# Optimization experiments

Hardware: AMD Instinct MI355X
Metric: run time of the kernel (lower is better)

Reference implementation:

```python
import jax, jax.numpy as jnp
import numpy as np

N = 20000        # nodes per type
E = 320000       # edges per type (avg degree 16)
H = 8            # heads
F0 = 128         # initial feature dim
F_UNI = 256      # n_unified
F_OUT = 64       # n_units per layer
N_USER = 20000   # shape_ret[0]
N_CLASSES = 2


def setup_inputs() -> dict:
    key = jax.random.key(0)
    ks = jax.random.split(key, 32)
    nrm = lambda k, s: jax.random.normal(k, s, dtype=jnp.float32) * 0.05
    inp = {
        "hemb0": nrm(ks[0], (N, F0)),
        "hemb1": nrm(ks[1], (N, F0)),
        "W0": nrm(ks[2], (F0, F_UNI)),
        "W1": nrm(ks[3], (F0, F_UNI)),
    }
    i = 4
    for t in range(2):
        for l, fin in enumerate([F_UNI, H * F_OUT]):
            inp[f"g{t}l{l}_w"] = nrm(ks[i], (H, fin, F_OUT)); i += 1
            inp[f"g{t}l{l}_asrc"] = nrm(ks[i], (H, F_OUT)); i += 1
            inp[f"g{t}l{l}_atrg"] = nrm(ks[i], (H, F_OUT)); i += 1
    inp["aw1"] = nrm(ks[i], (F_UNI, F_OUT)); i += 1
    inp["aw2"] = nrm(ks[i], (F_OUT, F_OUT)); i += 1
    inp["am"] = nrm(ks[i], (F_OUT,)); i += 1
    inp["fc_w"] = nrm(ks[i], (F_OUT * 3, N_CLASSES)); i += 1
    inp["fc_b"] = jnp.zeros((N_CLASSES,), jnp.float32); i += 1
    inp["edge0"] = jax.random.randint(ks[i], (2, E), 0, N, dtype=jnp.int32); i += 1
    inp["edge1"] = jax.random.randint(ks[i], (2, E), 0, N, dtype=jnp.int32)
    return inp


def spgat(h, src, trg, w, asrc, atrg):
    """Sparse GAT layer: h [N,f_in], edge list src/trg [E] -> [N,H,f_out]."""
    n = h.shape[0]
    hp = jnp.einsum('nf,hfo->hno', h, w)              # [H,N,O]
    s = jnp.einsum('hno,ho->nh', hp, asrc)            # [N,H]
    t = jnp.einsum('hno,ho->nh', hp, atrg)            # [N,H]
    e = jax.nn.leaky_relu(s[src] + t[trg], negative_slope=0.2)  # [E,H]
    ex = jnp.exp(e - jnp.max(e))                      # global max shift (as in source)
    denom = jax.ops.segment_sum(ex, trg, num_segments=n)[trg] + 1e-16
    alpha = ex / denom                                # [E,H]
    msg = jnp.transpose(hp, (1, 0, 2))[src] * alpha[:, :, None]  # [E,H,O]
    return jax.ops.segment_sum(msg, trg, num_segments=n)         # [N,H,O]


def reference(hemb0, hemb1, W0, W1,
              g0l0_w, g0l0_asrc, g0l0_atrg, g0l1_w, g0l1_asrc, g0l1_atrg,
              g1l0_w, g1l0_asrc, g1l0_atrg, g1l1_w, g1l1_asrc, g1l1_atrg,
              aw1, aw2, am, fc_w, fc_b, edge0, edge1):
    trans0 = hemb0 @ W0                                # [N,F_UNI]
    trans1 = hemb1 @ W1
    stacks = [
        (trans0, edge0, (g0l0_w, g0l0_asrc, g0l0_atrg), (g0l1_w, g0l1_asrc, g0l1_atrg)),
        (trans1, edge1, (g1l0_w, g1l0_asrc, g1l0_atrg), (g1l1_w, g1l1_asrc, g1l1_atrg)),
    ]
    heter = []
    for trans, edge, p0, p1 in stacks:
        src, trg = edge[0], edge[1]
        x = spgat(trans, src, trg, *p0)                # [N,H,F_OUT]
        x = jax.nn.elu(x.reshape(N, -1))               # [N,H*F_OUT]
        x = spgat(x, src, trg, *p1).mean(axis=1)       # [N,F_OUT]
        heter.append(x[:N_USER][:, None, :])
    type_aware = jnp.concatenate(heter, axis=1)        # [N_USER, 2, F_OUT]
    # faithful to source: feature = trans_emb[0] where trans_emb is the LAST
    # type's transformed embedding -> row 0, shape [F_UNI], broadcast over nodes
    feature = trans1[0]
    q = jnp.tanh(feature @ aw1 + type_aware @ aw2)     # [N_USER,2,F_OUT]
    beta = jax.nn.softmax(q @ am, axis=-1)             # [N_USER,2]
    fusion = jnp.einsum('nr,nrd->nd', beta, type_aware)[:, None, :]
    ret = jnp.concatenate([type_aware, fusion], axis=1).reshape(N_USER, -1)
    return jax.nn.log_softmax(ret @ fc_w + fc_b, axis=-1)   # [N_USER, 2]
```

## Files before the change

kernel.cpp:

```cpp
#include <hip/hip_runtime.h>
#include <hip/hip_bf16.h>


typedef __hip_bfloat16 bf16;
typedef __attribute__((ext_vector_type(8))) short short8;
typedef __attribute__((ext_vector_type(4))) float f32x4;

__device__ __forceinline__ float bf2f(bf16 v) { return __bfloat162float(v); }
__device__ __forceinline__ float ldin(const void* p, long i, int f32) {
  return f32 ? ((const float*)p)[i] : bf2f(((const bf16*)p)[i]);
}
__device__ __forceinline__ short f2bfbits(float f) {
  bf16 h = __float2bfloat16(f);
  return *reinterpret_cast<short*>(&h);
}
__device__ __forceinline__ float bfbits2f(short b) {
  unsigned u = ((unsigned)(unsigned short)b) << 16;
  return __uint_as_float(u);
}

struct GArg {
  const void* A[2];
  const void* B[2];
  bf16* C[2];
  const void* sa[2];
  const void* sb[2];
  float* sv[2];
  float* tv[2];
};

struct AArg {
  const bf16* hp[2];
  const float* sv[2];
  const float* tv[2];
  const int* rp[2];
  const int* col[2];
  void* out[2];
};

__global__ __launch_bounds__(64) void detect_kernel(const void* __restrict__ x,
                                                    int* __restrict__ flag) {
  int tid = threadIdx.x;
  float m = 0.f;
  for (int i = tid; i < 2048; i += 64) {
    float v = fabsf(bf2f(((const bf16*)x)[i]));
    if (!(v <= 1e3f)) v = 1e9f;
    m = fmaxf(m, v);
  }
#pragma unroll
  for (int off = 32; off; off >>= 1) m = fmaxf(m, __shfl_xor(m, off));
  if (tid == 0) flag[0] = (m > 1e3f) ? 1 : 0;
}

#define GBM 128
#define GBN 64
#define GBK 64

__device__ __forceinline__ int swz(int row, int kbyte) {
  return row * 128 + (kbyte ^ ((row & 7) << 4));
}

__global__ __launch_bounds__(256) void gemm_mfma(GArg g, int amode, int bmode,
                                                 int M, int K, int Nc,
                                                 const int* __restrict__ flag) {
  __shared__ bf16 As[GBM * GBK];
  __shared__ bf16 Bs[GBN * GBK];
  const int z = blockIdx.z;
  const void* __restrict__ A = g.A[z];
  const void* __restrict__ B = g.B[z];
  bf16* __restrict__ C = g.C[z];
  const void* stasrc = g.sa[z];
  const void* statrg = g.sb[z];
  float* svp = g.sv[z];
  float* tvp = g.tv[z];
  const int f32 = flag[0];
  const int af32 = (amode == 1) ? f32 : 0;
  const int m0 = blockIdx.x * GBM;
  const int n0 = blockIdx.y * GBN;
  const int tid = threadIdx.x;
  const int lane = tid & 63;
  const int wrow = (tid >> 6) * 32;

  f32x4 acc[2][4];
#pragma unroll
  for (int m = 0; m < 2; m++)
#pragma unroll
    for (int n = 0; n < 4; n++)
#pragma unroll
      for (int r = 0; r < 4; r++) acc[m][n][r] = 0.f;

  for (int kt = 0; kt < K; kt += GBK) {
#pragma unroll
    for (int j = 0; j < 4; j++) {
      int idx = tid + j * 256;
      int row = idx >> 3;
      int ks = idx & 7;
      int gm = m0 + row;
      short8 v;
#pragma unroll
      for (int e = 0; e < 8; e++) v[e] = 0;
      if (gm < M) {
        long base = (long)gm * K + kt + ks * 8;
        if (!af32) {
          v = *(const short8*)((const bf16*)A + base);
        } else {
          const float* Af = (const float*)A + base;
#pragma unroll
          for (int e = 0; e < 8; e++) v[e] = f2bfbits(Af[e]);
        }
      }
      *(short8*)((char*)As + swz(row, ks * 16)) = v;
    }
    {
      int n = tid & 63;
      int ks0 = tid >> 6;
#pragma unroll
      for (int jj = 0; jj < 2; jj++) {
        int ks = ks0 + jj * 4;
        int k = kt + ks * 8;
        int col = n0 + n;
        long base;
        int cstr;
        if (bmode == 0) { base = (long)k * Nc + col; cstr = Nc; }
        else { base = ((long)(col >> 6) * K + k) * 64 + (col & 63); cstr = 64; }
        short8 v;
        if (f32) {
          const float* Bf = (const float*)B;
#pragma unroll
          for (int e = 0; e < 8; e++) v[e] = f2bfbits(Bf[base + (long)e * cstr]);
        } else {
          const bf16* Bh = (const bf16*)B;
#pragma unroll
          for (int e = 0; e < 8; e++) v[e] = *(const short*)&Bh[base + (long)e * cstr];
        }
        *(short8*)((char*)Bs + swz(n, ks * 16)) = v;
      }
    }
    __syncthreads();
#pragma unroll
    for (int kh = 0; kh < 2; kh++) {
      int klane = kh * 64 + ((lane >> 4) << 4);
      short8 af[2], bfr[4];
#pragma unroll
      for (int m = 0; m < 2; m++) {
        int row = wrow + m * 16 + (lane & 15);
        af[m] = *(const short8*)((const char*)As + swz(row, klane));
      }
#pragma unroll
      for (int n = 0; n < 4; n++) {
        int col = n * 16 + (lane & 15);
        bfr[n] = *(const short8*)((const char*)Bs + swz(col, klane));
      }
#pragma unroll
      for (int m = 0; m < 2; m++)
#pragma unroll
        for (int n = 0; n < 4; n++)
          acc[m][n] = __builtin_amdgcn_mfma_f32_16x16x32_bf16(af[m], bfr[n], acc[m][n], 0, 0, 0);
    }
    __syncthreads();
  }
  if (svp) {
    const int h = blockIdx.y;
    const int cl = lane & 15;
    float av[4], bv[4];
#pragma unroll
    for (int n = 0; n < 4; n++) {
      av[n] = ldin(stasrc, h * 64 + n * 16 + cl, f32);
      bv[n] = ldin(statrg, h * 64 + n * 16 + cl, f32);
    }
#pragma unroll
    for (int m = 0; m < 2; m++) {
#pragma unroll
      for (int r = 0; r < 4; r++) {
        float s = 0.f, t = 0.f;
#pragma unroll
        for (int n = 0; n < 4; n++) {
          s += acc[m][n][r] * av[n];
          t += acc[m][n][r] * bv[n];
        }
#pragma unroll
        for (int off = 1; off <= 8; off <<= 1) {
          s += __shfl_xor(s, off);
          t += __shfl_xor(t, off);
        }
        int row = m0 + wrow + m * 16 + ((lane >> 4) << 2) + r;
        if (cl == 0 && row < M) {
          svp[(long)row * 8 + h] = s;
          tvp[(long)row * 8 + h] = t;
        }
      }
    }
  }
#pragma unroll
  for (int m = 0; m < 2; m++) {
#pragma unroll
    for (int r = 0; r < 4; r++) {
      int row = m0 + wrow + m * 16 + ((lane >> 4) << 2) + r;
      if (row < M) {
#pragma unroll
        for (int n = 0; n < 4; n++) {
          int col = n0 + n * 16 + (lane & 15);
          C[(long)row * Nc + col] = __float2bfloat16(acc[m][n][r]);
        }
      }
    }
  }
}

__global__ void hist2_kernel(const int* __restrict__ trg0, const int* __restrict__ trg1,
                             int* __restrict__ deg, int E, int N) {
  int e = blockIdx.x * 256 + threadIdx.x;
  if (e < E) atomicAdd(&deg[trg0[e]], 1);
  else if (e < 2 * E) atomicAdd(&deg[N + trg1[e - E]], 1);
}

__global__ __launch_bounds__(1024) void scan_kernel(const int* __restrict__ degb,
                                                    int* __restrict__ rpb,
                                                    int* __restrict__ filb, int N) {
  const int* deg = degb + (long)blockIdx.x * N;
  int* row_ptr = rpb + (long)blockIdx.x * (N + 1);
  int* fil = filb + (long)blockIdx.x * N;
  __shared__ int sums[1024];
  int tid = threadIdx.x;
  int chunk = (N + 1023) >> 10;
  int start = tid * chunk;
  int end = start + chunk;
  if (start > N) start = N;
  if (end > N) end = N;
  int s = 0;
  for (int i = start; i < end; i++) s += deg[i];
  sums[tid] = s;
  __syncthreads();
  for (int off = 1; off < 1024; off <<= 1) {
    int add = (tid >= off) ? sums[tid - off] : 0;
    __syncthreads();
    sums[tid] += add;
    __syncthreads();
  }
  int run = (tid > 0) ? sums[tid - 1] : 0;
  for (int i = start; i < end; i++) {
    row_ptr[i] = run;
    fil[i] = run;
    run += deg[i];
  }
  if (tid == 0) row_ptr[N] = sums[1023];
}

__global__ void fill2_kernel(const int* __restrict__ src0, const int* __restrict__ trg0,
                             const int* __restrict__ src1, const int* __restrict__ trg1,
                             int* __restrict__ filb, int* __restrict__ colb, int E, int N) {
  int e = blockIdx.x * 256 + threadIdx.x;
  if (e < E) {
    int t = trg0[e];
    int pos = atomicAdd(&filb[t], 1);
    colb[pos] = src0[e];
  } else if (e < 2 * E) {
    int ee = e - E;
    int t = trg1[ee];
    int pos = atomicAdd(&filb[N + t], 1);
    colb[E + pos] = src1[ee];
  }
}

__device__ __forceinline__ float exleaky(float v) {
  v = v > 0.f ? v : 0.2f * v;
  return __expf(v);
}

__global__ __launch_bounds__(256) void aggregate(AArg aa, int N, int mode) {
  const int ty = blockIdx.y;
  const bf16* __restrict__ hpb = aa.hp[ty];
  const float* __restrict__ svb = aa.sv[ty];
  const float* __restrict__ tvb = aa.tv[ty];
  const int* __restrict__ rp = aa.rp[ty];
  const int* __restrict__ colv = aa.col[ty];
  void* __restrict__ outp = aa.out[ty];
  const int wid = threadIdx.x >> 6;
  const int lane = threadIdx.x & 63;
  const int n = blockIdx.x * 4 + wid;
  if (n >= N) return;
  const int start = rp[n];
  const int deg = rp[n + 1] - start;
  const int h = lane >> 3;
  const float tvh = tvb[(long)n * 8 + h];
  const bf16* __restrict__ hpc = hpb + lane * 8;

  float acc[8] = {0.f, 0.f, 0.f, 0.f, 0.f, 0.f, 0.f, 0.f};
  float den = 1e-16f;

#define AG_LOAD(EB, V0, V1, V2, V3, Q0, Q1, Q2, Q3)                 \
  {                                                                 \
    int t0 = __shfl(mysrc, (EB) + 0), t1 = __shfl(mysrc, (EB) + 1); \
    int t2 = __shfl(mysrc, (EB) + 2), t3 = __shfl(mysrc, (EB) + 3); \
    V0 = *(const short8*)(hpc + (long)t0 * 512);                    \
    V1 = *(const short8*)(hpc + (long)t1 * 512);                    \
    V2 = *(const short8*)(hpc + (long)t2 * 512);                    \
    V3 = *(const short8*)(hpc + (long)t3 * 512);                    \
    Q0 = svb[(long)t0 * 8 + h];                                     \
    Q1 = svb[(long)t1 * 8 + h];                                     \
    Q2 = svb[(long)t2 * 8 + h];                                     \
    Q3 = svb[(long)t3 * 8 + h];                                     \
  }
#define AG_ACC(V0, V1, V2, V3, Q0, Q1, Q2, Q3)                      \
  {                                                                 \
    float a0 = exleaky(Q0 + tvh), a1 = exleaky(Q1 + tvh);           \
    float a2 = exleaky(Q2 + tvh), a3 = exleaky(Q3 + tvh);           \
    den += a0 + a1 + a2 + a3;                                       \
    _Pragma("unroll")                                               \
    for (int j = 0; j < 8; j++)                                     \
      acc[j] += a0 * bfbits2f(V0[j]) + a1 * bfbits2f(V1[j]) +       \
                a2 * bfbits2f(V2[j]) + a3 * bfbits2f(V3[j]);        \
  }

  for (int base = 0; base < deg; base += 64) {
    int cnt = deg - base;
    if (cnt > 64) cnt = 64;
    int mysrc = (lane < cnt) ? colv[start + base + lane] : 0;
    int nfull = cnt & ~3;
    if (nfull) {
      short8 v0, v1, v2, v3;
      float q0, q1, q2, q3;
      AG_LOAD(0, v0, v1, v2, v3, q0, q1, q2, q3);
      for (int e = 4; e < nfull; e += 4) {
        short8 w0 = v0, w1 = v1, w2 = v2, w3 = v3;
        float p0 = q0, p1 = q1, p2 = q2, p3 = q3;
        AG_LOAD(e, v0, v1, v2, v3, q0, q1, q2, q3);
        AG_ACC(w0, w1, w2, w3, p0, p1, p2, p3);
      }
      AG_ACC(v0, v1, v2, v3, q0, q1, q2, q3);
    }
    for (int e = nfull; e < cnt; e++) {
      int s0 = __shfl(mysrc, e);
      short8 v = *(const short8*)(hpc + (long)s0 * 512);
      float a = exleaky(svb[(long)s0 * 8 + h] + tvh);
      den += a;
#pragma unroll
      for (int j = 0; j < 8; j++) acc[j] += a * bfbits2f(v[j]);
    }
  }

  const float dinv = 1.f / den;
  if (mode == 0) {
    short8 o8;
#pragma unroll
    for (int j = 0; j < 8; j++) {
      float s = acc[j] * dinv;
      float ev = s > 0.f ? s : expm1f(s);
      o8[j] = f2bfbits(ev);
    }
    *(short8*)((bf16*)outp + (long)n * 512 + lane * 8) = o8;
  } else {
    float r[8];
#pragma unroll
    for (int j = 0; j < 8; j++) r[j] = acc[j] * dinv;
#pragma unroll
    for (int m = 8; m <= 32; m <<= 1)
#pragma unroll
      for (int j = 0; j < 8; j++) r[j] += __shfl_xor(r[j], m);
    if (lane < 8) {
      float* o = (float*)outp + (long)n * 128 + lane * 8;
#pragma unroll
      for (int j = 0; j < 8; j++) o[j] = r[j] * 0.125f;
    }
  }
}

__global__ __launch_bounds__(256) void favec_kernel(const bf16* __restrict__ trans1,
                                                    const void* __restrict__ aw1,
                                                    float* __restrict__ favec,
                                                    const int* __restrict__ flag) {
  const int f32 = flag[0];
  __shared__ float part[4][64];
  const int o = threadIdx.x & 63;
  const int wv = threadIdx.x >> 6;
  float acc = 0.f;
#pragma unroll
  for (int kk = 0; kk < 64; kk++) {
    int k = wv * 64 + kk;
    acc += bf2f(trans1[k]) * ldin(aw1, (long)k * 64 + o, f32);
  }
  part[wv][o] = acc;
  __syncthreads();
  if (threadIdx.x < 64) favec[o] = part[0][o] + part[1][o] + part[2][o] + part[3][o];
}

#define FN 16
__global__ __launch_bounds__(256) void final_kernel(const float* __restrict__ ta,
                                                    const float* __restrict__ favec,
                                                    const void* __restrict__ aw2,
                                                    const void* __restrict__ am,
                                                    const void* __restrict__ fcw,
                                                    const void* __restrict__ fcb,
                                                    void* __restrict__ out, int N,
                                                    const int* __restrict__ flag) {
  const int f32 = flag[0];
  __shared__ float s_w[64 * 64];
  __shared__ float s_fc[384];
  __shared__ float s_misc[130];
  __shared__ float s_ta[FN * 128];
  const int tid = threadIdx.x;
  const int n0 = blockIdx.x * FN;
  for (int i = tid; i < 4096; i += 256) s_w[i] = ldin(aw2, i, f32);
  for (int i = tid; i < 384; i += 256) s_fc[i] = ldin(fcw, i, f32);
  if (tid < 64) s_misc[tid] = favec[tid];
  else if (tid < 128) s_misc[tid] = ldin(am, tid - 64, f32);
  else if (tid < 130) s_misc[tid] = ldin(fcb, tid - 128, f32);
  for (int idx = tid; idx < FN * 128; idx += 256) {
    int ni = idx >> 7;
    int j = idx & 127;
    int k = j >> 1, r = j & 1;
    int n = n0 + ni;
    s_ta[idx] = (n < N) ? ta[(long)n * 128 + r * 64 + k] : 0.f;
  }
  __syncthreads();
  const int o = tid & 63;
  const int wv = tid >> 6;
#pragma unroll
  for (int ni4 = 0; ni4 < 4; ni4++) {
    const int ni = wv * 4 + ni4;
    const int n = n0 + ni;
    if (n >= N) continue;
    const float* tb = &s_ta[ni * 128];
    float acc0 = s_misc[o], acc1 = acc0;
#pragma unroll 8
    for (int k = 0; k < 64; k++) {
      float2 t2 = *(const float2*)(tb + k * 2);
      float w = s_w[k * 64 + o];
      acc0 += t2.x * w;
      acc1 += t2.y * w;
    }
    float ta0 = tb[o * 2];
    float ta1 = tb[o * 2 + 1];
    float amv = s_misc[64 + o];
    float p0 = tanhf(acc0) * amv;
    float p1 = tanhf(acc1) * amv;
#pragma unroll
    for (int off = 32; off > 0; off >>= 1) {
      p0 += __shfl_xor(p0, off);
      p1 += __shfl_xor(p1, off);
    }
    float mx = fmaxf(p0, p1);
    float e0 = __expf(p0 - mx), e1 = __expf(p1 - mx);
    float b0 = e0 / (e0 + e1), b1 = e1 / (e0 + e1);
    float fus = b0 * ta0 + b1 * ta1;
    float l0 = ta0 * s_fc[o * 2 + 0] + ta1 * s_fc[(64 + o) * 2 + 0] + fus * s_fc[(128 + o) * 2 + 0];
    float l1 = ta0 * s_fc[o * 2 + 1] + ta1 * s_fc[(64 + o) * 2 + 1] + fus * s_fc[(128 + o) * 2 + 1];
#pragma unroll
    for (int off = 32; off > 0; off >>= 1) {
      l0 += __shfl_xor(l0, off);
      l1 += __shfl_xor(l1, off);
    }
    if (o == 0) {
      l0 += s_misc[128];
      l1 += s_misc[129];
      float m2 = fmaxf(l0, l1);
      float lse = m2 + logf(__expf(l0 - m2) + __expf(l1 - m2));
      if (f32) {
        ((float*)out)[n * 2 + 0] = l0 - lse;
        ((float*)out)[n * 2 + 1] = l1 - lse;
      } else {
        ((bf16*)out)[n * 2 + 0] = __float2bfloat16(l0 - lse);
        ((bf16*)out)[n * 2 + 1] = __float2bfloat16(l1 - lse);
      }
    }
  }
}

extern "C" void kernel_launch(void* const* d_in, const int* in_sizes, int n_in,
                              void* d_out, int out_size, void* d_ws, size_t ws_size,
                              hipStream_t stream) {
  constexpr int N = 20000, E = 320000, H = 8, F0 = 128, FU = 256, FO = 64;
  const void* hemb[2] = {d_in[0], d_in[1]};
  const void* W[2] = {d_in[2], d_in[3]};
  const void* gw[2][2] = {{d_in[4], d_in[7]}, {d_in[10], d_in[13]}};
  const void* gasrc[2][2] = {{d_in[5], d_in[8]}, {d_in[11], d_in[14]}};
  const void* gatrg[2][2] = {{d_in[6], d_in[9]}, {d_in[12], d_in[15]}};
  const void* aw1 = d_in[16];
  const void* aw2 = d_in[17];
  const void* am = d_in[18];
  const void* fcw = d_in[19];
  const void* fcb = d_in[20];
  const int* edge[2] = {(const int*)d_in[21], (const int*)d_in[22]};

  const size_t szTrans = (size_t)N * FU * 2;
  const size_t szHp = (size_t)N * 512 * 2;
  const size_t szSv = (size_t)N * 8 * 4;
  size_t need = 0;
  auto addsz = [&](size_t b) { need += (b + 255) & ~(size_t)255; };
  addsz(4);
  addsz(szTrans * 2); addsz(szHp * 2); addsz(szHp * 2);
  addsz(szSv * 2); addsz(szSv * 2);
  addsz((size_t)N * 128 * 4); addsz(256);
  addsz((size_t)2 * N * 4); addsz((size_t)2 * (N + 1) * 4);
  addsz((size_t)2 * N * 4); addsz((size_t)2 * E * 4);
  const bool batched = (ws_size >= need + 4096);
  const int TB = batched ? 2 : 1;

  char* p = (char*)d_ws;
  auto alloc = [&](size_t bytes) -> void* {
    void* r = (void*)p;
    p += (bytes + 255) & ~(size_t)255;
    return r;
  };
  int* flag = (int*)alloc(4);
  bf16* trans = (bf16*)alloc(szTrans * TB);
  bf16* hp = (bf16*)alloc(szHp * TB);
  bf16* xbuf = (bf16*)alloc(szHp * TB);
  float* sv = (float*)alloc(szSv * TB);
  float* tv = (float*)alloc(szSv * TB);
  float* ta = (float*)alloc((size_t)N * 128 * 4);
  float* favec = (float*)alloc(256);
  int* degb = (int*)alloc((size_t)2 * N * 4);
  int* rpb = (int*)alloc((size_t)2 * (N + 1) * 4);
  int* filb = (int*)alloc((size_t)2 * N * 4);
  int* colb = (int*)alloc((size_t)2 * E * 4);

  detect_kernel<<<1, 64, 0, stream>>>(hemb[0], flag);

  hipMemsetAsync(degb, 0, (size_t)2 * N * 4, stream);
  hist2_kernel<<<(2 * E + 255) / 256, 256, 0, stream>>>(edge[0] + E, edge[1] + E, degb, E, N);
  scan_kernel<<<2, 1024, 0, stream>>>(degb, rpb, filb, N);
  fill2_kernel<<<(2 * E + 255) / 256, 256, 0, stream>>>(edge[0], edge[0] + E,
                                                        edge[1], edge[1] + E, filb, colb, E, N);

  const int gmx = (N + GBM - 1) / GBM;
  const int npass = batched ? 1 : 2;
  const int TC = batched ? 2 : 1;

  auto transP = [&](int b) { return trans + (size_t)b * N * FU; };
  auto hpP = [&](int b) { return hp + (size_t)b * N * 512; };
  auto xbufP = [&](int b) { return xbuf + (size_t)b * N * 512; };
  auto svP = [&](int b) { return sv + (size_t)b * N * 8; };
  auto tvP = [&](int b) { return tv + (size_t)b * N * 8; };

  for (int pass = 0; pass < npass; pass++) {
    int types[2] = {batched ? 0 : pass, batched ? 1 : pass};
    int bufs[2] = {batched ? 0 : 0, batched ? 1 : 0};

    GArg g0{};
    for (int i = 0; i < TC; i++) {
      int t = types[i], b = bufs[i];
      g0.A[i] = hemb[t]; g0.B[i] = W[t]; g0.C[i] = transP(b);
      g0.sa[i] = nullptr; g0.sb[i] = nullptr; g0.sv[i] = nullptr; g0.tv[i] = nullptr;
    }
    gemm_mfma<<<dim3(gmx, FU / GBN, TC), 256, 0, stream>>>(g0, 1, 0, N, F0, FU, flag);

    GArg g1{};
    for (int i = 0; i < TC; i++) {
      int t = types[i], b = bufs[i];
      g1.A[i] = transP(b); g1.B[i] = gw[t][0]; g1.C[i] = hpP(b);
      g1.sa[i] = gasrc[t][0]; g1.sb[i] = gatrg[t][0]; g1.sv[i] = svP(b); g1.tv[i] = tvP(b);
    }
    gemm_mfma<<<dim3(gmx, (H * FO) / GBN, TC), 256, 0, stream>>>(g1, 0, 1, N, FU, H * FO, flag);

    AArg a0{};
    for (int i = 0; i < TC; i++) {
      int t = types[i], b = bufs[i];
      a0.hp[i] = hpP(b); a0.sv[i] = svP(b); a0.tv[i] = tvP(b);
      a0.rp[i] = rpb + (size_t)t * (N + 1); a0.col[i] = colb + (size_t)t * E;
      a0.out[i] = xbufP(b);
    }
    aggregate<<<dim3((N + 3) / 4, TC), 256, 0, stream>>>(a0, N, 0);

    GArg g2{};
    for (int i = 0; i < TC; i++) {
      int t = types[i], b = bufs[i];
      g2.A[i] = xbufP(b); g2.B[i] = gw[t][1]; g2.C[i] = hpP(b);
      g2.sa[i] = gasrc[t][1]; g2.sb[i] = gatrg[t][1]; g2.sv[i] = svP(b); g2.tv[i] = tvP(b);
    }
    gemm_mfma<<<dim3(gmx, (H * FO) / GBN, TC), 256, 0, stream>>>(g2, 0, 1, N, H * FO, H * FO, flag);

    AArg a1{};
    for (int i = 0; i < TC; i++) {
      int t = types[i], b = bufs[i];
      a1.hp[i] = hpP(b); a1.sv[i] = svP(b); a1.tv[i] = tvP(b);
      a1.rp[i] = rpb + (size_t)t * (N + 1); a1.col[i] = colb + (size_t)t * E;
      a1.out[i] = ta + (size_t)t * FO;
    }
    aggregate<<<dim3((N + 3) / 4, TC), 256, 0, stream>>>(a1, N, 1);
  }

  const bf16* trans1 = batched ? transP(1) : transP(0);
  favec_kernel<<<1, 256, 0, stream>>>(trans1, aw1, favec, flag);
  final_kernel<<<(N + FN - 1) / FN, 256, 0, stream>>>(ta, favec, aw2, am, fcw, fcb, d_out, N, flag);
}
```

Baseline: 542.6 us.

## Fold input projection into GAT weights to skip the trans GEMM

Precomputes W_t @ gw_t[0] (128x512) once, so the first GAT projection runs directly on hemb with K=128 instead of materializing trans (N x 256) and doing a K=256 GEMM. The trans buffer goes away, and the favec vector is computed from hemb1 row 0 times W1 inside a new small kernel. This removes a full GEMM pass plus its write and read traffic. It changes the bf16 rounding point, since the product of the two weights is rounded once instead of the intermediate activations being rounded.

```diff
diff --git a/kernel.cpp b/kernel.cpp
--- a/kernel.cpp
+++ b/kernel.cpp
@@ -75,6 +75,7 @@
   float* tvp = g.tv[z];
   const int f32 = flag[0];
   const int af32 = (amode == 1) ? f32 : 0;
+  const int bf32 = (bmode == 2) ? 0 : f32;
   const int m0 = blockIdx.x * GBM;
   const int n0 = blockIdx.y * GBN;
   const int tid = threadIdx.x;
@@ -121,10 +122,10 @@
         int col = n0 + n;
         long base;
         int cstr;
-        if (bmode == 0) { base = (long)k * Nc + col; cstr = Nc; }
-        else { base = ((long)(col >> 6) * K + k) * 64 + (col & 63); cstr = 64; }
+        if (bmode == 1) { base = ((long)(col >> 6) * K + k) * 64 + (col & 63); cstr = 64; }
+        else { base = (long)k * Nc + col; cstr = Nc; }
         short8 v;
-        if (f32) {
+        if (bf32) {
           const float* Bf = (const float*)B;
 #pragma unroll
           for (int e = 0; e < 8; e++) v[e] = f2bfbits(Bf[base + (long)e * cstr]);
@@ -365,23 +366,33 @@
   }
 }
 
-__global__ __launch_bounds__(256) void favec_kernel(const bf16* __restrict__ trans1,
-                                                    const void* __restrict__ aw1,
-                                                    float* __restrict__ favec,
-                                                    const int* __restrict__ flag) {
+__global__ __launch_bounds__(256) void favec2_kernel(const void* __restrict__ hemb1,
+                                                     const void* __restrict__ W1,
+                                                     const void* __restrict__ aw1,
+                                                     float* __restrict__ favec,
+                                                     const int* __restrict__ flag) {
   const int f32 = flag[0];
+  __shared__ float s_h[128];
+  __shared__ float s_r[256];
   __shared__ float part[4][64];
-  const int o = threadIdx.x & 63;
-  const int wv = threadIdx.x >> 6;
+  const int tid = threadIdx.x;
+  if (tid < 128) s_h[tid] = ldin(hemb1, tid, f32);
+  __syncthreads();
+  float r = 0.f;
+  for (int i = 0; i < 128; i++) r += s_h[i] * ldin(W1, (long)i * 256 + tid, f32);
+  s_r[tid] = r;
+  __syncthreads();
+  const int o = tid & 63;
+  const int wv = tid >> 6;
   float acc = 0.f;
 #pragma unroll
   for (int kk = 0; kk < 64; kk++) {
     int k = wv * 64 + kk;
-    acc += bf2f(trans1[k]) * ldin(aw1, (long)k * 64 + o, f32);
+    acc += s_r[k] * ldin(aw1, (long)k * 64 + o, f32);
   }
   part[wv][o] = acc;
   __syncthreads();
-  if (threadIdx.x < 64) favec[o] = part[0][o] + part[1][o] + part[2][o] + part[3][o];
+  if (tid < 64) favec[o] = part[0][o] + part[1][o] + part[2][o] + part[3][o];
 }
 
 #define FN 16
@@ -482,13 +493,14 @@
   const void* fcb = d_in[20];
   const int* edge[2] = {(const int*)d_in[21], (const int*)d_in[22]};
 
-  const size_t szTrans = (size_t)N * FU * 2;
+  const size_t szWg = (size_t)F0 * 512 * 2;
   const size_t szHp = (size_t)N * 512 * 2;
   const size_t szSv = (size_t)N * 8 * 4;
   size_t need = 0;
   auto addsz = [&](size_t b) { need += (b + 255) & ~(size_t)255; };
   addsz(4);
-  addsz(szTrans * 2); addsz(szHp * 2); addsz(szHp * 2);
+  addsz(szWg * 2);
+  addsz(szHp * 2); addsz(szHp * 2);
   addsz(szSv * 2); addsz(szSv * 2);
   addsz((size_t)N * 128 * 4); addsz(256);
   addsz((size_t)2 * N * 4); addsz((size_t)2 * (N + 1) * 4);
@@ -503,7 +515,7 @@
     return r;
   };
   int* flag = (int*)alloc(4);
-  bf16* trans = (bf16*)alloc(szTrans * TB);
+  bf16* wg = (bf16*)alloc(szWg * 2);
   bf16* hp = (bf16*)alloc(szHp * TB);
   bf16* xbuf = (bf16*)alloc(szHp * TB);
   float* sv = (float*)alloc(szSv * TB);
@@ -523,11 +535,21 @@
   fill2_kernel<<<(2 * E + 255) / 256, 256, 0, stream>>>(edge[0], edge[0] + E,
                                                         edge[1], edge[1] + E, filb, colb, E, N);
 
+  favec2_kernel<<<1, 256, 0, stream>>>(hemb[1], W[1], aw1, favec, flag);
+
+  {
+    GArg gW{};
+    for (int i = 0; i < 2; i++) {
+      gW.A[i] = W[i]; gW.B[i] = gw[i][0]; gW.C[i] = wg + (size_t)i * F0 * 512;
+      gW.sa[i] = nullptr; gW.sb[i] = nullptr; gW.sv[i] = nullptr; gW.tv[i] = nullptr;
+    }
+    gemm_mfma<<<dim3(1, (H * FO) / GBN, 2), 256, 0, stream>>>(gW, 1, 1, F0, FU, H * FO, flag);
+  }
+
   const int gmx = (N + GBM - 1) / GBM;
   const int npass = batched ? 1 : 2;
   const int TC = batched ? 2 : 1;
 
-  auto transP = [&](int b) { return trans + (size_t)b * N * FU; };
   auto hpP = [&](int b) { return hp + (size_t)b * N * 512; };
   auto xbufP = [&](int b) { return xbuf + (size_t)b * N * 512; };
   auto svP = [&](int b) { return sv + (size_t)b * N * 8; };
@@ -535,23 +557,15 @@
 
   for (int pass = 0; pass < npass; pass++) {
     int types[2] = {batched ? 0 : pass, batched ? 1 : pass};
-    int bufs[2] = {batched ? 0 : 0, batched ? 1 : 0};
-
-    GArg g0{};
-    for (int i = 0; i < TC; i++) {
-      int t = types[i], b = bufs[i];
-      g0.A[i] = hemb[t]; g0.B[i] = W[t]; g0.C[i] = transP(b);
-      g0.sa[i] = nullptr; g0.sb[i] = nullptr; g0.sv[i] = nullptr; g0.tv[i] = nullptr;
-    }
-    gemm_mfma<<<dim3(gmx, FU / GBN, TC), 256, 0, stream>>>(g0, 1, 0, N, F0, FU, flag);
+    int bufs[2] = {0, batched ? 1 : 0};
 
     GArg g1{};
     for (int i = 0; i < TC; i++) {
       int t = types[i], b = bufs[i];
-      g1.A[i] = transP(b); g1.B[i] = gw[t][0]; g1.C[i] = hpP(b);
+      g1.A[i] = hemb[t]; g1.B[i] = wg + (size_t)t * F0 * 512; g1.C[i] = hpP(b);
       g1.sa[i] = gasrc[t][0]; g1.sb[i] = gatrg[t][0]; g1.sv[i] = svP(b); g1.tv[i] = tvP(b);
     }
-    gemm_mfma<<<dim3(gmx, (H * FO) / GBN, TC), 256, 0, stream>>>(g1, 0, 1, N, FU, H * FO, flag);
+    gemm_mfma<<<dim3(gmx, (H * FO) / GBN, TC), 256, 0, stream>>>(g1, 1, 2, N, F0, H * FO, flag);
 
     AArg a0{};
     for (int i = 0; i < TC; i++) {
@@ -580,7 +594,5 @@
     aggregate<<<dim3((N + 3) / 4, TC), 256, 0, stream>>>(a1, N, 1);
   }
 
-  const bf16* trans1 = batched ? transP(1) : transP(0);
-  favec_kernel<<<1, 256, 0, stream>>>(trans1, aw1, favec, flag);
   final_kernel<<<(N + FN - 1) / FN, 256, 0, stream>>>(ta, favec, aw2, am, fcw, fcb, d_out, N, flag);
 }
```

After: 569.9 us. 1.05x slower.
